# Optimization experiments

Measured on AMD Instinct MI355X. Metric: run time of the kernel, lower is better.

Reference implementation:

```python
import jax, jax.numpy as jnp
import numpy as np

R = 6
P = 2 * R + 1          # 13, correlation patch size
N = P * P              # 169 displacements
C = 32                 # one-hot label channels
FOUR_LN2 = 4.0 * float(np.log(2.0))


def _extract_windows(x, h, w):
    """Zero-pad by R and extract all PxP shifted views.
    x: (b, c, h, w) -> (b, c, N, h, w), displacement index n = dy*P + dx,
    matching both SpatialCorrelationSampler patch ordering and F.unfold."""
    xp = jnp.pad(x, ((0, 0), (0, 0), (R, R), (R, R)))
    return jnp.stack([xp[:, :, dy:dy + h, dx:dx + w]
                      for dy in range(P) for dx in range(P)], axis=2)


def setup_inputs():
    key = jax.random.key(0)
    k1, k2, k3 = jax.random.split(key, 3)
    feats_r = jax.random.normal(k1, (2, 2, 128, 64, 64), dtype=jnp.float32)
    feats_t = jax.random.normal(k2, (2, 128, 64, 64), dtype=jnp.float32)
    quantized_r = jax.random.randint(k3, (2, 2, 1, 256, 256), 0, C)
    return {"feats_r": feats_r, "feats_t": feats_t, "quantized_r": quantized_r}


def reference(feats_r, feats_t, quantized_r):
    nref, b, c, h, w = feats_r.shape
    hw = h * w

    # ---- local PxP correlation volume per reference (SpatialCorrelationSampler, k=1) ----
    corrs = []
    for i in range(nref):
        win = _extract_windows(feats_r[i], h, w)                       # (b,c,N,h,w)
        corrs.append(jnp.einsum('bchw,bcnhw->bnhw', feats_t, win).reshape(b, N, hw))
    corr = jax.nn.softmax(jnp.concatenate(corrs, axis=1), axis=1)      # (b, nref*N, hw)

    # ---- compact_verify: top-2 + gaussian heatmap refinement ----
    cc = corr.reshape(b, nref, N, hw).transpose(0, 1, 3, 2).reshape(b, nref * hw, N)
    ccd = jax.lax.stop_gradient(cc)                                     # torch uses .detach()
    vals, idx = jax.lax.top_k(ccd, 2)                                   # (b, L, 2)
    wts = jax.nn.softmax(vals, axis=-1)
    ys = (idx // P).astype(jnp.float32)
    xs = (idx % P).astype(jnp.float32)
    grid = jnp.arange(P, dtype=jnp.float32)
    dx = grid[None, None, None, :] - xs[..., None]                      # (b,L,2,P)
    dy = grid[None, None, None, :] - ys[..., None]                      # (b,L,2,P)
    heat = jnp.exp(-FOUR_LN2 * (dx[:, :, :, None, :] ** 2 + dy[:, :, :, :, None] ** 2))  # (b,L,2,P,P) [yy,xx]
    corr_heat = jnp.einsum('blkn,blk->bln', heat.reshape(b, nref * hw, 2, N), wts)
    vmax = jnp.max(vals, axis=-1, keepdims=True)
    corr2 = jnp.where(vmax > 0.1, corr_heat, cc)                        # mask/refine
    corr2 = corr2.reshape(b, nref, hw, N).transpose(0, 1, 3, 2).reshape(b, nref * N, hw)

    # ---- get_out: unfold one-hot reference labels and weighted-sum over window ----
    scale = quantized_r.shape[-2] // h                                  # prep: stride subsample
    ufs = []
    for i in range(nref):
        lab = quantized_r[i, :, 0, ::scale, ::scale]                    # (b,h,w)
        oh = jnp.transpose(jax.nn.one_hot(lab, C, dtype=feats_t.dtype), (0, 3, 1, 2))
        ufs.append(_extract_windows(oh, h, w).reshape(b, C, N, hw))
    image_uf = jnp.concatenate(ufs, axis=2)                             # (b,C,nref*N,hw)
    image_uf = image_uf.at[:, 1:].multiply(1.15)                        # inference boost
    out = jnp.einsum('bnl,bcnl->bcl', corr2, image_uf)
    return out.reshape(b, C, h, w)
```

## Files before the change

### kernel.cpp

```cpp
#include <hip/hip_runtime.h>
#include <math.h>

namespace {

constexpr int RAD  = 6;
constexpr int P    = 13;
constexpr int NWIN = 169;
constexpr int NTOT = 338;
constexpr int NCH  = 128;
constexpr int NCLS = 32;
constexpr int W    = 64;
constexpr int HW   = 4096;
constexpr float FOUR_LN2 = 2.772588722239781f;

constexpr int TX    = 32;
constexpr int CHUNK = 8;
constexpr int PW    = 48;
constexpr int PR    = 13;
constexpr int FRELEMS = CHUNK * PR * PW;
constexpr int NCHUNK  = NCH / CHUNK;
constexpr int TILE    = TX * NWIN;

__device__ __forceinline__ bool better(float va, int ia, float vb, int ib) {
  return (va > vb) || ((va == vb) && (ia < ib));
}

__global__ __launch_bounds__(256, 4) void corr_kernel(
    const float* __restrict__ fr,
    const float* __restrict__ ft,
    float* __restrict__ vol) {
  const int blk = blockIdx.x;
  const int xh = blk & 1;
  const int y  = (blk >> 1) & 63;
  const int bi = blk >> 7;
  const int b  = bi >> 1;
  const int ii = bi & 1;
  const int x0 = xh * TX;
  const int t  = threadIdx.x;
  const int cg = t >> 7;
  const int tl = t & 127;

  __shared__ __align__(16) float smem[2 * FRELEMS];
  __shared__ __align__(16) float ftbuf[2][CHUNK * TX];

  const int xg = tl & 7;
  const int dy = tl >> 3;
  const bool comp = (tl < 104);

  const float* frbase = fr + (size_t)((ii * 2 + b) * NCH) * HW;
  const float* ftbase = ft + (size_t)(b * NCH) * HW + y * W + x0;

  float acc[13][4];
  #pragma unroll
  for (int dx = 0; dx < 13; ++dx)
    #pragma unroll
    for (int k = 0; k < 4; ++k) acc[dx][k] = 0.f;

  float rg[20];
  float rft;

  auto stage_load = [&](int c0) {
    #pragma unroll
    for (int u = 0; u < 20; ++u) {
      const int e = t + u * 256;
      float v = 0.f;
      if (e < FRELEMS) {
        const int cc  = e / (PR * PW);
        const int rem = e - cc * (PR * PW);
        const int r   = rem / PW;
        const int xc  = rem - r * PW;
        const int yy  = y + r - RAD;
        const int xx  = x0 - RAD + xc;
        if ((unsigned)yy < 64u && (unsigned)xx < 64u && xc < 44)
          v = frbase[(size_t)(c0 + cc) * HW + yy * W + xx];
      }
      rg[u] = v;
    }
    const int cc = t >> 5;
    const int xl = t & 31;
    rft = ftbase[(size_t)(c0 + cc) * HW + xl];
  };
  auto stage_write = [&](int s) {
    float* frb = smem + s * FRELEMS;
    #pragma unroll
    for (int u = 0; u < 20; ++u) {
      const int e = t + u * 256;
      if (e < FRELEMS) frb[e] = rg[u];
    }
    ftbuf[s][t] = rft;
  };

  stage_load(0);
  stage_write(0);
  __syncthreads();

  for (int k = 0; k < NCHUNK; ++k) {
    const int cur = k & 1;
    if (k < NCHUNK - 1) stage_load((k + 1) * CHUNK);
    if (comp) {
      const float* frb = smem + cur * FRELEMS;
      #pragma unroll
      for (int c2 = 0; c2 < 4; ++c2) {
        const int cc = cg * 4 + c2;
        const float* fp = frb + (cc * PR + dy) * PW + xg * 4;
        float w[16];
        #pragma unroll
        for (int j = 0; j < 4; ++j) {
          const float4 q4 = *(const float4*)(fp + 4 * j);
          w[4 * j] = q4.x; w[4 * j + 1] = q4.y; w[4 * j + 2] = q4.z; w[4 * j + 3] = q4.w;
        }
        const float4 tq = *(const float4*)(&ftbuf[cur][cc * TX + xg * 4]);
        const float tqa[4] = {tq.x, tq.y, tq.z, tq.w};
        #pragma unroll
        for (int dx = 0; dx < 13; ++dx)
          #pragma unroll
          for (int kk = 0; kk < 4; ++kk)
            acc[dx][kk] = fmaf(w[dx + kk], tqa[kk], acc[dx][kk]);
      }
    }
    __syncthreads();
    if (k < NCHUNK - 1) stage_write(cur ^ 1);
    __syncthreads();
  }

  if (comp && cg == 1) {
    float* rb = smem + tl * 52;
    #pragma unroll
    for (int dx = 0; dx < 13; ++dx)
      *(float4*)(rb + dx * 4) = make_float4(acc[dx][0], acc[dx][1], acc[dx][2], acc[dx][3]);
  }
  __syncthreads();
  if (comp && cg == 0) {
    const float* rb = smem + tl * 52;
    #pragma unroll
    for (int dx = 0; dx < 13; ++dx) {
      const float4 r = *(const float4*)(rb + dx * 4);
      acc[dx][0] += r.x; acc[dx][1] += r.y; acc[dx][2] += r.z; acc[dx][3] += r.w;
    }
  }
  __syncthreads();
  if (comp && cg == 0) {
    #pragma unroll
    for (int dx = 0; dx < 13; ++dx)
      #pragma unroll
      for (int kk = 0; kk < 4; ++kk)
        smem[(xg * 4 + kk) * NWIN + dy * 13 + dx] = acc[dx][kk];
  }
  __syncthreads();
  {
    float* gb = vol + ((size_t)(b * HW + y * W + x0) * 2 + ii) * NWIN;
    for (int u = 0; u < 22; ++u) {
      const int e = t + u * 256;
      if (e < TILE) {
        const int xl2 = e / NWIN;
        const int mm  = e - xl2 * NWIN;
        gb[(size_t)xl2 * (2 * NWIN) + mm] = smem[e];
      }
    }
  }
}

__global__ __launch_bounds__(256) void lab_kernel(
    const int* __restrict__ q, int* __restrict__ lab) {
  const int idx = blockIdx.x * 256 + threadIdx.x;
  const int i2b = idx >> 12;
  const int rem = idx & 4095;
  const int yy  = rem >> 6;
  const int xx  = rem & 63;
  lab[idx] = q[(size_t)i2b * 65536 + (yy * 4) * 256 + xx * 4];
}

__global__ __launch_bounds__(256) void post_kernel(
    const float* __restrict__ vol,
    const int*  __restrict__ lab,
    float* __restrict__ out) {
  const int blk  = blockIdx.x;
  const int t    = threadIdx.x;
  const int w    = t >> 6;
  const int lane = t & 63;
  const int pix  = blk * 4 + w;
  const int b = pix >> 12;
  const int y = (pix >> 6) & 63;
  const int x = pix & 63;

  __shared__ float accS[4][NCLS];
  accS[w][lane & 31] = 0.f;

  float vv[6];
  float lmax = -INFINITY;
  const float* vp = vol + (size_t)pix * NTOT;
  #pragma unroll
  for (int k = 0; k < 6; ++k) {
    const int e = lane + 64 * k;
    vv[k] = (e < NTOT) ? vp[e] : -INFINITY;
    lmax = fmaxf(lmax, vv[k]);
  }
  #pragma unroll
  for (int off = 32; off > 0; off >>= 1)
    lmax = fmaxf(lmax, __shfl_xor(lmax, off));

  float p[6];
  float lsum = 0.f;
  #pragma unroll
  for (int k = 0; k < 6; ++k) {
    const int e = lane + 64 * k;
    p[k] = (e < NTOT) ? __expf(vv[k] - lmax) : 0.f;
    lsum += p[k];
  }
  #pragma unroll
  for (int off = 32; off > 0; off >>= 1)
    lsum += __shfl_xor(lsum, off);
  const float rinv = 1.f / lsum;
  #pragma unroll
  for (int k = 0; k < 6; ++k) p[k] *= rinv;

  float a1_0 = -1.f, a2_0 = -1.f, a1_1 = -1.f, a2_1 = -1.f;
  int   j1_0 = 1 << 20, j2_0 = 1 << 20, j1_1 = 1 << 20, j2_1 = 1 << 20;
  #pragma unroll
  for (int k = 0; k < 6; ++k) {
    const int e = lane + 64 * k;
    if (e < NTOT) {
      const int r = (e >= NWIN) ? 1 : 0;
      const int m = e - r * NWIN;
      const float pv = p[k];
      if (r == 0) {
        if (better(pv, m, a1_0, j1_0)) { a2_0 = a1_0; j2_0 = j1_0; a1_0 = pv; j1_0 = m; }
        else if (better(pv, m, a2_0, j2_0)) { a2_0 = pv; j2_0 = m; }
      } else {
        if (better(pv, m, a1_1, j1_1)) { a2_1 = a1_1; j2_1 = j1_1; a1_1 = pv; j1_1 = m; }
        else if (better(pv, m, a2_1, j2_1)) { a2_1 = pv; j2_1 = m; }
      }
    }
  }
  #pragma unroll
  for (int off = 32; off > 0; off >>= 1) {
    {
      const float u1 = __shfl_xor(a1_0, off); const int q1 = __shfl_xor(j1_0, off);
      const float u2 = __shfl_xor(a2_0, off); const int q2 = __shfl_xor(j2_0, off);
      if (better(u1, q1, a1_0, j1_0)) {
        float nv2; int ni2;
        if (better(a1_0, j1_0, u2, q2)) { nv2 = a1_0; ni2 = j1_0; }
        else                            { nv2 = u2;   ni2 = q2; }
        a1_0 = u1; j1_0 = q1; a2_0 = nv2; j2_0 = ni2;
      } else if (better(u1, q1, a2_0, j2_0)) { a2_0 = u1; j2_0 = q1; }
    }
    {
      const float u1 = __shfl_xor(a1_1, off); const int q1 = __shfl_xor(j1_1, off);
      const float u2 = __shfl_xor(a2_1, off); const int q2 = __shfl_xor(j2_1, off);
      if (better(u1, q1, a1_1, j1_1)) {
        float nv2; int ni2;
        if (better(a1_1, j1_1, u2, q2)) { nv2 = a1_1; ni2 = j1_1; }
        else                            { nv2 = u2;   ni2 = q2; }
        a1_1 = u1; j1_1 = q1; a2_1 = nv2; j2_1 = ni2;
      } else if (better(u1, q1, a2_1, j2_1)) { a2_1 = u1; j2_1 = q1; }
    }
  }

  const float e10 = __expf(a1_0), e20 = __expf(a2_0);
  const float rs0 = 1.f / (e10 + e20);
  const float w00 = e10 * rs0, w10 = e20 * rs0;
  const bool  fl0 = (a1_0 > 0.1f);
  const float xs00 = (float)(j1_0 % P), ys00 = (float)(j1_0 / P);
  const float xs10 = (float)(j2_0 % P), ys10 = (float)(j2_0 / P);

  const float e11 = __expf(a1_1), e21 = __expf(a2_1);
  const float rs1 = 1.f / (e11 + e21);
  const float w01 = e11 * rs1, w11 = e21 * rs1;
  const bool  fl1 = (a1_1 > 0.1f);
  const float xs01 = (float)(j1_1 % P), ys01 = (float)(j1_1 / P);
  const float xs11 = (float)(j2_1 % P), ys11 = (float)(j2_1 / P);

  #pragma unroll
  for (int k = 0; k < 6; ++k) {
    const int e = lane + 64 * k;
    if (e < NTOT) {
      const int r  = (e >= NWIN) ? 1 : 0;
      const int m  = e - r * NWIN;
      const int dy = m / P;
      const int dx = m - dy * P;
      const bool  fl = r ? fl1 : fl0;
      float val;
      if (fl) {
        const float wA = r ? w01 : w00, wB = r ? w11 : w10;
        const float xA = r ? xs01 : xs00, yA = r ? ys01 : ys00;
        const float xB = r ? xs11 : xs10, yB = r ? ys11 : ys10;
        const float fdx0 = (float)dx - xA, fdy0 = (float)dy - yA;
        const float fdx1 = (float)dx - xB, fdy1 = (float)dy - yB;
        val = wA * __expf(-FOUR_LN2 * (fdx0 * fdx0 + fdy0 * fdy0))
            + wB * __expf(-FOUR_LN2 * (fdx1 * fdx1 + fdy1 * fdy1));
      } else {
        val = p[k];
      }
      const int yy = y + dy - RAD;
      const int xx = x + dx - RAD;
      if ((unsigned)yy < 64u && (unsigned)xx < 64u) {
        const int cls = lab[(size_t)(r * 2 + b) * 4096 + yy * W + xx];
        atomicAdd(&accS[w][cls], val);
      }
    }
  }
  __syncthreads();

  if (t < 4 * NCLS) {
    const int cls = t >> 2;
    const int j   = t & 3;
    const int x0  = (blk * 4) & 63;
    const float sc = (cls == 0) ? 1.0f : 1.15f;
    out[(size_t)(b * NCLS + cls) * HW + y * W + x0 + j] = accS[j][cls] * sc;
  }
}

}

extern "C" void kernel_launch(void* const* d_in, const int* in_sizes, int n_in,
                              void* d_out, int out_size, void* d_ws, size_t ws_size,
                              hipStream_t stream) {
  const float* fr = (const float*)d_in[0];
  const float* ft = (const float*)d_in[1];
  const int*   q  = (const int*)d_in[2];
  float* out = (float*)d_out;
  float* vol = (float*)d_ws;
  int*   lab = (int*)((char*)d_ws + (size_t)2 * HW * NTOT * sizeof(float));

  lab_kernel<<<dim3(64), dim3(256), 0, stream>>>(q, lab);
  corr_kernel<<<dim3(2 * 2 * 64 * 2), dim3(256), 0, stream>>>(fr, ft, vol);
  post_kernel<<<dim3(2 * HW / 4), dim3(256), 0, stream>>>(vol, lab, out);
}
```

Before: 61.61 us.

## Pre-pad reference features so correlation kernel loads tiles with unguarded float4

A new pad kernel writes a zero-padded (76x80) copy of the reference features and also extracts the subsampled labels, replacing the separate label kernel. The correlation kernel then stages each chunk with a few vectorized float4 loads at precomputed offsets instead of many bounds-checked scalar loads, and one barrier per chunk is removed. The launch bound is relaxed from 4 to 2 blocks per SM. The cost is an extra full pass writing about 12MB of padded data, and lower guaranteed occupancy.

```diff
diff --git a/kernel.cpp b/kernel.cpp
--- a/kernel.cpp
+++ b/kernel.cpp
@@ -13,20 +13,54 @@
 constexpr int HW   = 4096;
 constexpr float FOUR_LN2 = 2.772588722239781f;
 
+constexpr int PADH = 76;
+constexpr int PADW = 80;
+constexpr int PADCH = PADH * PADW;
+
 constexpr int TX    = 32;
 constexpr int CHUNK = 8;
 constexpr int PW    = 48;
 constexpr int PR    = 13;
 constexpr int FRELEMS = CHUNK * PR * PW;
-constexpr int NCHUNK  = NCH / CHUNK;
-constexpr int TILE    = TX * NWIN;
+constexpr int NV4   = FRELEMS / 4;
+constexpr int NCHUNK = NCH / CHUNK;
+constexpr int TILE  = TX * NWIN;
+constexpr size_t VOLF = (size_t)2 * HW * NTOT;
 
 __device__ __forceinline__ bool better(float va, int ia, float vb, int ib) {
   return (va > vb) || ((va == vb) && (ia < ib));
 }
 
-__global__ __launch_bounds__(256, 4) void corr_kernel(
-    const float* __restrict__ fr,
+__global__ __launch_bounds__(256) void pad_kernel(
+    const float* __restrict__ fr, const int* __restrict__ q,
+    float* __restrict__ frp, int* __restrict__ lab) {
+  const int gid = blockIdx.x * 256 + threadIdx.x;
+  const int xx4 = gid % 20;
+  const int row = gid / 20;
+  const int yy  = row % PADH;
+  const int cr  = row / PADH;
+  const int ly  = yy - 6;
+  float4 v;
+  float* vp = (float*)&v;
+  const float* src = fr + (size_t)cr * HW + ly * W;
+  #pragma unroll
+  for (int j = 0; j < 4; ++j) {
+    const int lx = xx4 * 4 + j - 6;
+    vp[j] = ((unsigned)ly < 64u && (unsigned)lx < 64u) ? src[lx] : 0.f;
+  }
+  *(float4*)(frp + (size_t)gid * 4) = v;
+
+  if (gid < 16384) {
+    const int i2b = gid >> 12;
+    const int rem = gid & 4095;
+    const int y2  = rem >> 6;
+    const int x2  = rem & 63;
+    lab[gid] = q[(size_t)i2b * 65536 + (y2 * 4) * 256 + x2 * 4];
+  }
+}
+
+__global__ __launch_bounds__(256, 2) void corr_kernel(
+    const float* __restrict__ frp,
     const float* __restrict__ ft,
     float* __restrict__ vol) {
   const int blk = blockIdx.x;
@@ -46,9 +80,21 @@
   const int xg = tl & 7;
   const int dy = tl >> 3;
   const bool comp = (tl < 104);
-
-  const float* frbase = fr + (size_t)((ii * 2 + b) * NCH) * HW;
-  const float* ftbase = ft + (size_t)(b * NCH) * HW + y * W + x0;
+  const bool tail = (t < NV4 - 1024);
+
+  const float* frpbase = frp + (size_t)((ii * 2 + b) * NCH) * PADCH;
+  const float* ftp4 = ft + (size_t)(b * NCH + (t >> 3)) * HW + y * W + x0 + (t & 7) * 4;
+
+  int off4[5];
+  #pragma unroll
+  for (int u = 0; u < 5; ++u) {
+    const int e4 = t + u * 256;
+    const int cc  = e4 / 156;
+    const int rem = e4 - cc * 156;
+    const int r   = rem / 12;
+    const int xc4 = rem - r * 12;
+    off4[u] = cc * PADCH + (y + r) * PADW + x0 + xc4 * 4;
+  }
 
   float acc[13][4];
   #pragma unroll
@@ -56,38 +102,22 @@
     #pragma unroll
     for (int k = 0; k < 4; ++k) acc[dx][k] = 0.f;
 
-  float rg[20];
-  float rft;
+  float4 rg4[5];
+  float4 rft4;
 
   auto stage_load = [&](int c0) {
-    #pragma unroll
-    for (int u = 0; u < 20; ++u) {
-      const int e = t + u * 256;
-      float v = 0.f;
-      if (e < FRELEMS) {
-        const int cc  = e / (PR * PW);
-        const int rem = e - cc * (PR * PW);
-        const int r   = rem / PW;
-        const int xc  = rem - r * PW;
-        const int yy  = y + r - RAD;
-        const int xx  = x0 - RAD + xc;
-        if ((unsigned)yy < 64u && (unsigned)xx < 64u && xc < 44)
-          v = frbase[(size_t)(c0 + cc) * HW + yy * W + xx];
-      }
-      rg[u] = v;
-    }
-    const int cc = t >> 5;
-    const int xl = t & 31;
-    rft = ftbase[(size_t)(c0 + cc) * HW + xl];
+    const float* fb = frpbase + (size_t)c0 * PADCH;
+    #pragma unroll
+    for (int u = 0; u < 5; ++u)
+      if (u < 4 || tail) rg4[u] = *(const float4*)(fb + off4[u]);
+    if (t < 64) rft4 = *(const float4*)(ftp4 + (size_t)c0 * HW);
   };
   auto stage_write = [&](int s) {
     float* frb = smem + s * FRELEMS;
     #pragma unroll
-    for (int u = 0; u < 20; ++u) {
-      const int e = t + u * 256;
-      if (e < FRELEMS) frb[e] = rg[u];
-    }
-    ftbuf[s][t] = rft;
+    for (int u = 0; u < 5; ++u)
+      if (u < 4 || tail) *(float4*)(frb + (t + u * 256) * 4) = rg4[u];
+    if (t < 64) *(float4*)(&ftbuf[s][(t >> 3) * TX + (t & 7) * 4]) = rft4;
   };
 
   stage_load(0);
@@ -118,7 +148,6 @@
             acc[dx][kk] = fmaf(w[dx + kk], tqa[kk], acc[dx][kk]);
       }
     }
-    __syncthreads();
     if (k < NCHUNK - 1) stage_write(cur ^ 1);
     __syncthreads();
   }
@@ -158,16 +187,6 @@
       }
     }
   }
-}
-
-__global__ __launch_bounds__(256) void lab_kernel(
-    const int* __restrict__ q, int* __restrict__ lab) {
-  const int idx = blockIdx.x * 256 + threadIdx.x;
-  const int i2b = idx >> 12;
-  const int rem = idx & 4095;
-  const int yy  = rem >> 6;
-  const int xx  = rem & 63;
-  lab[idx] = q[(size_t)i2b * 65536 + (yy * 4) * 256 + xx * 4];
 }
 
 __global__ __launch_bounds__(256) void post_kernel(
@@ -320,9 +339,10 @@
   const int*   q  = (const int*)d_in[2];
   float* out = (float*)d_out;
   float* vol = (float*)d_ws;
-  int*   lab = (int*)((char*)d_ws + (size_t)2 * HW * NTOT * sizeof(float));
-
-  lab_kernel<<<dim3(64), dim3(256), 0, stream>>>(q, lab);
-  corr_kernel<<<dim3(2 * 2 * 64 * 2), dim3(256), 0, stream>>>(fr, ft, vol);
+  float* frp = (float*)((char*)d_ws + VOLF * sizeof(float));
+  int*   lab = (int*)((char*)frp + (size_t)4 * NCH * PADCH * sizeof(float));
+
+  pad_kernel<<<dim3(3040), dim3(256), 0, stream>>>(fr, q, frp, lab);
+  corr_kernel<<<dim3(2 * 2 * 64 * 2), dim3(256), 0, stream>>>(frp, ft, vol);
   post_kernel<<<dim3(2 * HW / 4), dim3(256), 0, stream>>>(vol, lab, out);
 }
```

Measured after the change: 84.66 us. +37.4%, slower.
